# Kernel optimization log

Hardware: AMD Instinct MI355X
Metric: run time of the kernel (lower is better)

## Reference

```python
import jax, jax.numpy as jnp
import numpy as np

N = 8192          # num nodes
E = 262144        # num edges
F_IN = 512        # dataset.num_features
HID = 256         # hidden_dim
C = 16            # dataset.num_classes
ALPHA = 1.0
GAMMA = 1.0
EPS = 0.4
LN_EPS = 1e-5


def setup_inputs() -> dict:
    key = jax.random.key(0)
    ks = jax.random.split(key, 16)
    x = jax.random.normal(ks[0], (N, F_IN), dtype=jnp.float32)
    edge_index = jax.random.randint(ks[1], (2, E), 0, N, dtype=jnp.int64)
    def lin(k, fan_in, fan_out):
        s = 1.0 / np.sqrt(fan_in)
        return jax.random.uniform(k, (fan_in, fan_out), jnp.float32, -s, s)
    return {
        "x": x,
        "edge_index": edge_index,
        "W0": lin(ks[2], F_IN, HID), "b0": jnp.zeros((HID,), jnp.float32),
        "ln0_g": jnp.ones((HID,), jnp.float32), "ln0_b": jnp.zeros((HID,), jnp.float32),
        "W1": lin(ks[3], HID, HID), "b1": jnp.zeros((HID,), jnp.float32),
        "ln1_g": jnp.ones((HID,), jnp.float32), "ln1_b": jnp.zeros((HID,), jnp.float32),
        "W2": lin(ks[4], HID, C), "b2": jnp.zeros((C,), jnp.float32),
    }


def _layernorm(h, g, b):
    mu = jnp.mean(h, axis=-1, keepdims=True)
    var = jnp.var(h, axis=-1, keepdims=True)
    return (h - mu) * jax.lax.rsqrt(var + LN_EPS) * g + b


def _hpf_weight_matrix(edge_index, n, dtype):
    # to_dense_adj with parallel-edge accumulation
    A = jnp.zeros((n, n), dtype).at[edge_index[0], edge_index[1]].add(jnp.asarray(1.0, dtype))
    eye = jnp.eye(n, dtype=dtype)
    A = GAMMA * A + ALPHA * eye
    # D^{-1/2} A D^{-1/2} as fused row/col scaling (same math as the two diag matmuls)
    dinv = jax.lax.rsqrt(jnp.sum(A, axis=1))
    A_hat = dinv[:, None] * A * dinv[None, :]
    # (eps - 1) I + (I - A_hat) == eps*I - A_hat ; keep only positive entries (edge extraction)
    U = EPS * eye - A_hat
    return jnp.where(U > 0, U, jnp.asarray(0.0, dtype))


def reference(x, edge_index, W0, b0, ln0_g, ln0_b, W1, b1, ln1_g, ln1_b, W2, b2):
    Wmat = _hpf_weight_matrix(edge_index, x.shape[0], x.dtype)
    # GCNConv(normalize=False): h' = scatter_{src->tgt}(w * (h@W)[src]) + bias == Wmat^T @ (h@W) + b
    def gcn(h, W, b):
        return Wmat.T @ (h @ W) + b
    h = gcn(x, W0, b0)
    h = _layernorm(jax.nn.relu(h), ln0_g, ln0_b)   # dropout p=0.0 -> identity
    h = gcn(h, W1, b1)
    h = _layernorm(jax.nn.relu(h), ln1_g, ln1_b)
    embedding = gcn(h, W2, b2)
    return embedding, jax.nn.log_softmax(embedding, axis=1)
```

## Files before the change

kernel.cpp:

```cpp
#include <hip/hip_runtime.h>

#define NN 8192
#define NE 262144
#define FIN 512
#define HIDN 256
#define NC 16
#define NHB 48

typedef __attribute__((ext_vector_type(8))) short bf16x8;
typedef __attribute__((ext_vector_type(4))) short bf16x4;
typedef __attribute__((ext_vector_type(4))) float f32x4;

static __device__ __forceinline__ unsigned short f2bf(float f) {
    union { float f; unsigned u; } v; v.f = f;
    unsigned r = v.u + 0x7FFFu + ((v.u >> 16) & 1u);
    return (unsigned short)(r >> 16);
}

template<int K, int N>
static __device__ __forceinline__ void pack_w(const float* __restrict__ W,
                                              unsigned short* __restrict__ Wp, int f) {
    constexpr int KC = K / 32;
    int lane = f & 63;
    int g = f >> 6;
    int kc = g % KC;
    int nt = g / KC;
    int n = nt * 16 + (lane & 15);
    int kbase = kc * 32 + (lane >> 4) * 8;
    bf16x8 v;
#pragma unroll
    for (int j = 0; j < 8; ++j) v[j] = (short)f2bf(W[(kbase + j) * N + n]);
    *(bf16x8*)&Wp[f * 8] = v;
}

__global__ __launch_bounds__(512) void work_kernel(
    const int* __restrict__ ei,
    const float* __restrict__ W0, const float* __restrict__ W1, const float* __restrict__ W2,
    int* __restrict__ cnt, int* __restrict__ partial,
    unsigned short* __restrict__ Wp0, unsigned short* __restrict__ Wp1,
    unsigned short* __restrict__ Wp2)
{
    __shared__ int hist[NN];
    const int tid = threadIdx.x, bid = blockIdx.x;
    if (bid < NHB) {
#pragma unroll
        for (int i = 0; i < NN / 512; ++i) hist[tid + i * 512] = 0;
        __syncthreads();
        const int4* s4 = (const int4*)ei;
        const int4* t4 = (const int4*)(ei + NE);
        const int p = bid * 512 + tid;
#pragma unroll
        for (int i = 0; i < 3; ++i) {
            int c = p + i * (NHB * 512);
            if (c < NE / 4) {
                int4 s = s4[c];
                int4 t = t4[c];
                atomicAdd(&hist[s.x], 1);
                atomicAdd(&hist[s.y], 1);
                atomicAdd(&hist[s.z], 1);
                atomicAdd(&hist[s.w], 1);
                if (s.x == t.x) atomicAdd(&cnt[NN + s.x], 1);
                if (s.y == t.y) atomicAdd(&cnt[NN + s.y], 1);
                if (s.z == t.z) atomicAdd(&cnt[NN + s.z], 1);
                if (s.w == t.w) atomicAdd(&cnt[NN + s.w], 1);
            }
        }
        __syncthreads();
#pragma unroll
        for (int i = 0; i < NN / 512; ++i)
            partial[bid * NN + tid + i * 512] = hist[tid + i * 512];
    } else {
        int gp = (bid - NHB) * 512 + tid;
        if (gp < 16384)       pack_w<512, 256>(W0, Wp0, gp);
        else if (gp < 24576)  pack_w<256, 256>(W1, Wp1, gp - 16384);
        else                  pack_w<256, 16 >(W2, Wp2, gp - 24576);
    }
}

static __device__ __forceinline__ void ln_epilogue(
    const f32x4 acc[2][2], const float* __restrict__ bias, const float* __restrict__ gam,
    const float* __restrict__ bet, const float wdr[2][4],
    int w, int quad, int l16,
    unsigned short* sH, float red[][16])
{
    float bv[2], gv[2], btv[2];
#pragma unroll
    for (int nt = 0; nt < 2; ++nt) {
        int col = w * 32 + nt * 16 + l16;
        bv[nt] = bias[col]; gv[nt] = gam[col]; btv[nt] = bet[col];
    }
    float vv[2][2][4], s[2][4], ss[2][4];
#pragma unroll
    for (int mt = 0; mt < 2; ++mt)
#pragma unroll
        for (int reg = 0; reg < 4; ++reg) {
            float ps = 0.f, pss = 0.f;
#pragma unroll
            for (int nt = 0; nt < 2; ++nt) {
                float v = fmaxf(fmaf(wdr[mt][reg], acc[mt][nt][reg], bv[nt]), 0.f);
                vv[mt][nt][reg] = v;
                ps += v; pss += v * v;
            }
            s[mt][reg] = ps; ss[mt][reg] = pss;
        }
#pragma unroll
    for (int off = 1; off < 16; off <<= 1)
#pragma unroll
        for (int mt = 0; mt < 2; ++mt)
#pragma unroll
            for (int reg = 0; reg < 4; ++reg) {
                s[mt][reg]  += __shfl_xor(s[mt][reg],  off, 64);
                ss[mt][reg] += __shfl_xor(ss[mt][reg], off, 64);
            }
    if (l16 == 0) {
#pragma unroll
        for (int mt = 0; mt < 2; ++mt)
#pragma unroll
            for (int reg = 0; reg < 4; ++reg) {
                int rl = mt * 16 + quad * 4 + reg;
                red[rl][w * 2]     = s[mt][reg];
                red[rl][w * 2 + 1] = ss[mt][reg];
            }
    }
    __syncthreads();
#pragma unroll
    for (int mt = 0; mt < 2; ++mt)
#pragma unroll
        for (int reg = 0; reg < 4; ++reg) {
            int rl = mt * 16 + quad * 4 + reg;
            float ts = 0.f, tss = 0.f;
#pragma unroll
            for (int i = 0; i < 8; ++i) { ts += red[rl][2 * i]; tss += red[rl][2 * i + 1]; }
            float mu  = ts * (1.0f / 256.0f);
            float var = tss * (1.0f / 256.0f) - mu * mu;
            float rs  = rsqrtf(var + 1e-5f);
#pragma unroll
            for (int nt = 0; nt < 2; ++nt) {
                float o = (vv[mt][nt][reg] - mu) * rs * gv[nt] + btv[nt];
                sH[rl * 264 + w * 32 + nt * 16 + l16] = f2bf(o);
            }
        }
    __syncthreads();
}

__global__ __launch_bounds__(512) void mega_kernel(
    const float* __restrict__ x,
    const unsigned short* __restrict__ Wp0, const unsigned short* __restrict__ Wp1,
    const unsigned short* __restrict__ Wp2,
    const float* __restrict__ b0, const float* __restrict__ g0, const float* __restrict__ be0,
    const float* __restrict__ b1, const float* __restrict__ g1, const float* __restrict__ be1,
    const float* __restrict__ b2, const int* __restrict__ cnt,
    const int* __restrict__ partial,
    float* __restrict__ out)
{
    __shared__ unsigned short sX[32 * 520];
    __shared__ unsigned short sH[32 * 264];
    __shared__ float red[32][16];
    __shared__ float swd[32];

    const int tid  = threadIdx.x;
    const int lane = tid & 63, w = tid >> 6;
    const int quad = lane >> 4, l16 = lane & 15;
    const int row0 = blockIdx.x * 32;

    const float4* x4 = (const float4*)x;
    float4 v[8];
#pragma unroll
    for (int i = 0; i < 4; ++i) {
        int idx = i * 1024 + tid * 2;
        v[2 * i]     = x4[row0 * 128 + idx];
        v[2 * i + 1] = x4[row0 * 128 + idx + 1];
    }

    if (tid < 32) {
        int d = 0;
#pragma unroll
        for (int b = 0; b < NHB; ++b) d += partial[b * NN + row0 + tid];
        int base = cnt[2 * NN];
        int sl = cnt[NN + row0 + tid] - base;
        float u = 0.4f - (1.0f + (float)sl) / (1.0f + (float)d);
        swd[tid] = u > 0.0f ? u : 0.0f;
    }

#pragma unroll
    for (int i = 0; i < 4; ++i) {
        int idx = i * 1024 + tid * 2;
        int r = idx >> 7, c4 = idx & 127;
        bf16x8 h;
        h[0] = (short)f2bf(v[2 * i].x);     h[1] = (short)f2bf(v[2 * i].y);
        h[2] = (short)f2bf(v[2 * i].z);     h[3] = (short)f2bf(v[2 * i].w);
        h[4] = (short)f2bf(v[2 * i + 1].x); h[5] = (short)f2bf(v[2 * i + 1].y);
        h[6] = (short)f2bf(v[2 * i + 1].z); h[7] = (short)f2bf(v[2 * i + 1].w);
        *(bf16x8*)&sX[r * 520 + c4 * 4] = h;
    }
    __syncthreads();

    float wdr[2][4];
#pragma unroll
    for (int mt = 0; mt < 2; ++mt)
#pragma unroll
        for (int reg = 0; reg < 4; ++reg) wdr[mt][reg] = swd[mt * 16 + quad * 4 + reg];

    const bf16x8* Wp0v = (const bf16x8*)Wp0;
    const bf16x8* Wp1v = (const bf16x8*)Wp1;
    const bf16x8* Wp2v = (const bf16x8*)Wp2;

    f32x4 acc[2][2];
#pragma unroll
    for (int mt = 0; mt < 2; ++mt)
#pragma unroll
        for (int nt = 0; nt < 2; ++nt) acc[mt][nt] = (f32x4){0.f, 0.f, 0.f, 0.f};
#pragma unroll
    for (int kc = 0; kc < 16; ++kc) {
        bf16x8 a0 = *(const bf16x8*)&sX[l16 * 520        + kc * 32 + quad * 8];
        bf16x8 a1 = *(const bf16x8*)&sX[(16 + l16) * 520 + kc * 32 + quad * 8];
#pragma unroll
        for (int nt = 0; nt < 2; ++nt) {
            bf16x8 b = Wp0v[((w * 2 + nt) * 16 + kc) * 64 + lane];
            acc[0][nt] = __builtin_amdgcn_mfma_f32_16x16x32_bf16(a0, b, acc[0][nt], 0, 0, 0);
            acc[1][nt] = __builtin_amdgcn_mfma_f32_16x16x32_bf16(a1, b, acc[1][nt], 0, 0, 0);
        }
    }
    ln_epilogue(acc, b0, g0, be0, wdr, w, quad, l16, sH, red);

    f32x4 acc1[2][2];
#pragma unroll
    for (int mt = 0; mt < 2; ++mt)
#pragma unroll
        for (int nt = 0; nt < 2; ++nt) acc1[mt][nt] = (f32x4){0.f, 0.f, 0.f, 0.f};
#pragma unroll
    for (int kc = 0; kc < 8; ++kc) {
        bf16x8 a0 = *(const bf16x8*)&sH[l16 * 264        + kc * 32 + quad * 8];
        bf16x8 a1 = *(const bf16x8*)&sH[(16 + l16) * 264 + kc * 32 + quad * 8];
#pragma unroll
        for (int nt = 0; nt < 2; ++nt) {
            bf16x8 b = Wp1v[((w * 2 + nt) * 8 + kc) * 64 + lane];
            acc1[0][nt] = __builtin_amdgcn_mfma_f32_16x16x32_bf16(a0, b, acc1[0][nt], 0, 0, 0);
            acc1[1][nt] = __builtin_amdgcn_mfma_f32_16x16x32_bf16(a1, b, acc1[1][nt], 0, 0, 0);
        }
    }
    ln_epilogue(acc1, b1, g1, be1, wdr, w, quad, l16, sH, red);

    if (w < 2) {
        f32x4 acch = (f32x4){0.f, 0.f, 0.f, 0.f};
#pragma unroll
        for (int kc = 0; kc < 8; ++kc) {
            bf16x8 a = *(const bf16x8*)&sH[(w * 16 + l16) * 264 + kc * 32 + quad * 8];
            bf16x8 b = Wp2v[kc * 64 + lane];
            acch = __builtin_amdgcn_mfma_f32_16x16x32_bf16(a, b, acch, 0, 0, 0);
        }
        float bb = b2[l16];
#pragma unroll
        for (int reg = 0; reg < 4; ++reg) {
            int row = row0 + w * 16 + quad * 4 + reg;
            float v2 = fmaf(wdr[w][reg], acch[reg], bb);
            float m = v2;
#pragma unroll
            for (int off = 8; off >= 1; off >>= 1) m = fmaxf(m, __shfl_xor(m, off, 64));
            float e = __expf(v2 - m);
            float se = e;
#pragma unroll
            for (int off = 8; off >= 1; off >>= 1) se += __shfl_xor(se, off, 64);
            float lsm = (v2 - m) - __logf(se);
            out[row * 16 + l16] = v2;
            out[NN * 16 + row * 16 + l16] = lsm;
        }
    }
}

extern "C" void kernel_launch(void* const* d_in, const int* in_sizes, int n_in,
                              void* d_out, int out_size, void* d_ws, size_t ws_size,
                              hipStream_t stream) {
    const float* x  = (const float*)d_in[0];
    const int*   ei = (const int*)d_in[1];
    const float* W0 = (const float*)d_in[2];
    const float* b0 = (const float*)d_in[3];
    const float* g0 = (const float*)d_in[4];
    const float* be0 = (const float*)d_in[5];
    const float* W1 = (const float*)d_in[6];
    const float* b1 = (const float*)d_in[7];
    const float* g1 = (const float*)d_in[8];
    const float* be1 = (const float*)d_in[9];
    const float* W2 = (const float*)d_in[10];
    const float* b2 = (const float*)d_in[11];
    float* out = (float*)d_out;

    char* ws = (char*)d_ws;
    int*            cnt = (int*)ws;
    unsigned short* Wp0 = (unsigned short*)(ws + 68 * 1024);
    unsigned short* Wp1 = (unsigned short*)(ws + 324 * 1024);
    unsigned short* Wp2 = (unsigned short*)(ws + 452 * 1024);
    int*        partial = (int*)(ws + 460 * 1024);

    work_kernel<<<NHB + 49, 512, 0, stream>>>(ei, W0, W1, W2, cnt, partial, Wp0, Wp1, Wp2);
    mega_kernel<<<NN / 32, 512, 0, stream>>>(x, Wp0, Wp1, Wp2,
                                             b0, g0, be0, b1, g1, be1, b2, cnt, partial, out);
}
```

Measured before the change: 101.4 us.

## Split X staging into halves and prefetch weight fragments before epilogues

The X tile load is split into two column halves. The first half is converted to bf16 and its MFMA k-steps run while the second half's conversion is still pending, which adds an extra barrier. The first two k-chunks of each layer's packed weights are also loaded into registers ahead of time (before the x conversion and before each LayerNorm epilogue), so global-load latency overlaps with other work. This increases register pressure and may lower occupancy.

After: 101.8 us. Within noise of the previous version (+0.4%).

```diff
diff --git a/kernel.cpp b/kernel.cpp
--- a/kernel.cpp
+++ b/kernel.cpp
@@ -163,14 +163,29 @@
     const int quad = lane >> 4, l16 = lane & 15;
     const int row0 = blockIdx.x * 32;
 
+    const bf16x8* Wp0v = (const bf16x8*)Wp0;
+    const bf16x8* Wp1v = (const bf16x8*)Wp1;
+    const bf16x8* Wp2v = (const bf16x8*)Wp2;
+
     const float4* x4 = (const float4*)x;
     float4 v[8];
 #pragma unroll
-    for (int i = 0; i < 4; ++i) {
-        int idx = i * 1024 + tid * 2;
-        v[2 * i]     = x4[row0 * 128 + idx];
-        v[2 * i + 1] = x4[row0 * 128 + idx + 1];
-    }
+    for (int p = 0; p < 2; ++p) {
+        int idx = p * 1024 + tid * 2;
+        int r = idx >> 6, c4 = idx & 63;
+        const float4* base = &x4[(row0 + r) * 128 + c4];
+        v[2 * p]         = base[0];
+        v[2 * p + 1]     = base[1];
+        v[4 + 2 * p]     = base[64];
+        v[4 + 2 * p + 1] = base[65];
+    }
+
+    bf16x8 b0r[2][2];
+#pragma unroll
+    for (int kc = 0; kc < 2; ++kc)
+#pragma unroll
+        for (int nt = 0; nt < 2; ++nt)
+            b0r[kc][nt] = Wp0v[((w * 2 + nt) * 16 + kc) * 64 + lane];
 
     if (tid < 32) {
         int d = 0;
@@ -183,14 +198,14 @@
     }
 
 #pragma unroll
-    for (int i = 0; i < 4; ++i) {
-        int idx = i * 1024 + tid * 2;
-        int r = idx >> 7, c4 = idx & 127;
+    for (int p = 0; p < 2; ++p) {
+        int idx = p * 1024 + tid * 2;
+        int r = idx >> 6, c4 = idx & 63;
         bf16x8 h;
-        h[0] = (short)f2bf(v[2 * i].x);     h[1] = (short)f2bf(v[2 * i].y);
-        h[2] = (short)f2bf(v[2 * i].z);     h[3] = (short)f2bf(v[2 * i].w);
-        h[4] = (short)f2bf(v[2 * i + 1].x); h[5] = (short)f2bf(v[2 * i + 1].y);
-        h[6] = (short)f2bf(v[2 * i + 1].z); h[7] = (short)f2bf(v[2 * i + 1].w);
+        h[0] = (short)f2bf(v[2 * p].x);     h[1] = (short)f2bf(v[2 * p].y);
+        h[2] = (short)f2bf(v[2 * p].z);     h[3] = (short)f2bf(v[2 * p].w);
+        h[4] = (short)f2bf(v[2 * p + 1].x); h[5] = (short)f2bf(v[2 * p + 1].y);
+        h[6] = (short)f2bf(v[2 * p + 1].z); h[7] = (short)f2bf(v[2 * p + 1].w);
         *(bf16x8*)&sX[r * 520 + c4 * 4] = h;
     }
     __syncthreads();
@@ -201,17 +216,39 @@
 #pragma unroll
         for (int reg = 0; reg < 4; ++reg) wdr[mt][reg] = swd[mt * 16 + quad * 4 + reg];
 
-    const bf16x8* Wp0v = (const bf16x8*)Wp0;
-    const bf16x8* Wp1v = (const bf16x8*)Wp1;
-    const bf16x8* Wp2v = (const bf16x8*)Wp2;
-
     f32x4 acc[2][2];
 #pragma unroll
     for (int mt = 0; mt < 2; ++mt)
 #pragma unroll
         for (int nt = 0; nt < 2; ++nt) acc[mt][nt] = (f32x4){0.f, 0.f, 0.f, 0.f};
 #pragma unroll
-    for (int kc = 0; kc < 16; ++kc) {
+    for (int kc = 0; kc < 8; ++kc) {
+        bf16x8 a0 = *(const bf16x8*)&sX[l16 * 520        + kc * 32 + quad * 8];
+        bf16x8 a1 = *(const bf16x8*)&sX[(16 + l16) * 520 + kc * 32 + quad * 8];
+#pragma unroll
+        for (int nt = 0; nt < 2; ++nt) {
+            bf16x8 b = (kc < 2) ? b0r[kc][nt]
+                                : Wp0v[((w * 2 + nt) * 16 + kc) * 64 + lane];
+            acc[0][nt] = __builtin_amdgcn_mfma_f32_16x16x32_bf16(a0, b, acc[0][nt], 0, 0, 0);
+            acc[1][nt] = __builtin_amdgcn_mfma_f32_16x16x32_bf16(a1, b, acc[1][nt], 0, 0, 0);
+        }
+    }
+
+#pragma unroll
+    for (int p = 0; p < 2; ++p) {
+        int idx = p * 1024 + tid * 2;
+        int r = idx >> 6, c4 = idx & 63;
+        bf16x8 h;
+        h[0] = (short)f2bf(v[4 + 2 * p].x);     h[1] = (short)f2bf(v[4 + 2 * p].y);
+        h[2] = (short)f2bf(v[4 + 2 * p].z);     h[3] = (short)f2bf(v[4 + 2 * p].w);
+        h[4] = (short)f2bf(v[4 + 2 * p + 1].x); h[5] = (short)f2bf(v[4 + 2 * p + 1].y);
+        h[6] = (short)f2bf(v[4 + 2 * p + 1].z); h[7] = (short)f2bf(v[4 + 2 * p + 1].w);
+        *(bf16x8*)&sX[r * 520 + 256 + c4 * 4] = h;
+    }
+    __syncthreads();
+
+#pragma unroll
+    for (int kc = 8; kc < 16; ++kc) {
         bf16x8 a0 = *(const bf16x8*)&sX[l16 * 520        + kc * 32 + quad * 8];
         bf16x8 a1 = *(const bf16x8*)&sX[(16 + l16) * 520 + kc * 32 + quad * 8];
 #pragma unroll
@@ -221,6 +258,14 @@
             acc[1][nt] = __builtin_amdgcn_mfma_f32_16x16x32_bf16(a1, b, acc[1][nt], 0, 0, 0);
         }
     }
+
+    bf16x8 b1r[2][2];
+#pragma unroll
+    for (int kc = 0; kc < 2; ++kc)
+#pragma unroll
+        for (int nt = 0; nt < 2; ++nt)
+            b1r[kc][nt] = Wp1v[((w * 2 + nt) * 8 + kc) * 64 + lane];
+
     ln_epilogue(acc, b0, g0, be0, wdr, w, quad, l16, sH, red);
 
     f32x4 acc1[2][2];
@@ -234,11 +279,19 @@
         bf16x8 a1 = *(const bf16x8*)&sH[(16 + l16) * 264 + kc * 32 + quad * 8];
 #pragma unroll
         for (int nt = 0; nt < 2; ++nt) {
-            bf16x8 b = Wp1v[((w * 2 + nt) * 8 + kc) * 64 + lane];
+            bf16x8 b = (kc < 2) ? b1r[kc][nt]
+                                : Wp1v[((w * 2 + nt) * 8 + kc) * 64 + lane];
             acc1[0][nt] = __builtin_amdgcn_mfma_f32_16x16x32_bf16(a0, b, acc1[0][nt], 0, 0, 0);
             acc1[1][nt] = __builtin_amdgcn_mfma_f32_16x16x32_bf16(a1, b, acc1[1][nt], 0, 0, 0);
         }
     }
+
+    bf16x8 b2r[2];
+    if (w < 2) {
+#pragma unroll
+        for (int kc = 0; kc < 2; ++kc) b2r[kc] = Wp2v[kc * 64 + lane];
+    }
+
     ln_epilogue(acc1, b1, g1, be1, wdr, w, quad, l16, sH, red);
 
     if (w < 2) {
@@ -246,7 +299,7 @@
 #pragma unroll
         for (int kc = 0; kc < 8; ++kc) {
             bf16x8 a = *(const bf16x8*)&sH[(w * 16 + l16) * 264 + kc * 32 + quad * 8];
-            bf16x8 b = Wp2v[kc * 64 + lane];
+            bf16x8 b = (kc < 2) ? b2r[kc] : Wp2v[kc * 64 + lane];
             acch = __builtin_amdgcn_mfma_f32_16x16x32_bf16(a, b, acch, 0, 0, 0);
         }
         float bb = b2[l16];
```
